# Performance work log

Measured on AMD Instinct MI355X. Metric: run time of the kernel, lower is better.

Reference implementation:

```python
import jax, jax.numpy as jnp
import numpy as np

ATOM_FDIM = 133
BOND_FDIM = 147
HIDDEN = 300
DEPTH = 3
N_ATOMS = 100000
N_BONDS = 200000
MAX_NB = 6
N_MOLS = 4000


def setup_inputs() -> dict:
    key = jax.random.key(0)
    ks = jax.random.split(key, 10)
    f_atoms = jax.random.normal(ks[0], (N_ATOMS, ATOM_FDIM), dtype=jnp.float32)
    f_bonds = jax.random.normal(ks[1], (N_BONDS, BOND_FDIM), dtype=jnp.float32)
    a2b = jax.random.randint(ks[2], (N_ATOMS, MAX_NB), 0, N_BONDS)
    b2a = jax.random.randint(ks[3], (N_BONDS,), 0, N_ATOMS)
    b2revb = jax.random.randint(ks[4], (N_BONDS,), 0, N_BONDS)
    atom2mol = jnp.sort(jax.random.randint(ks[5], (N_ATOMS,), 0, N_MOLS))
    s = 1.0 / np.sqrt(HIDDEN)
    W_i = jax.random.uniform(ks[6], (BOND_FDIM, HIDDEN), jnp.float32, -s, s)
    W_h = jax.random.uniform(ks[7], (HIDDEN, HIDDEN), jnp.float32, -s, s)
    W_o_w = jax.random.uniform(ks[8], (ATOM_FDIM + HIDDEN, HIDDEN), jnp.float32, -s, s)
    W_o_b = jax.random.uniform(ks[9], (HIDDEN,), jnp.float32, -s, s)
    return {"f_atoms": f_atoms, "f_bonds": f_bonds, "a2b": a2b, "b2a": b2a,
            "b2revb": b2revb, "atom2mol": atom2mol, "W_i": W_i, "W_h": W_h,
            "W_o_w": W_o_w, "W_o_b": W_o_b}


def reference(f_atoms, f_bonds, a2b, b2a, b2revb, atom2mol, W_i, W_h, W_o_w, W_o_b):
    # input = W_i(f_bonds); message = act(input)
    inp = f_bonds @ W_i                      # [n_bonds, hidden]
    message = jax.nn.relu(inp)
    for _ in range(DEPTH - 1):
        # gather neighbor bond messages per atom and sum: [n_atoms, max_nb, h] -> [n_atoms, h]
        a_message = message[a2b].sum(axis=1)
        rev_message = message[b2revb]        # [n_bonds, hidden]
        message = a_message[b2a] - rev_message
        message = jax.nn.relu(inp + message @ W_h)
    # final atom-level aggregation
    a_message = message[a2b].sum(axis=1)     # [n_atoms, hidden]
    a_input = jnp.concatenate([f_atoms, a_message], axis=1)
    atom_hiddens = jax.nn.relu(a_input @ W_o_w + W_o_b)
    # segment mean pooling over molecules
    sums = jax.ops.segment_sum(atom_hiddens, atom2mol, num_segments=N_MOLS)
    counts = jax.ops.segment_sum(jnp.ones((atom_hiddens.shape[0],), atom_hiddens.dtype),
                                 atom2mol, num_segments=N_MOLS)
    mol_vecs = sums / jnp.maximum(counts, 1.0)[:, None]  # zero vec for empty mols
    return mol_vecs
```

## Files before the change

kernel.cpp:

```cpp
#include <hip/hip_runtime.h>
#include <stdint.h>

#define ATOM_FDIM 133
#define BOND_FDIM 147
#define HIDDEN    300
#define N_ATOMS   100000
#define N_BONDS   200000
#define MAX_NB    6
#define N_MOLS    4000

#define KP_I 160
#define KP_H 320
#define KP_O 448
#define LDA  304
#define CPR  38

#define TM   128
#define ACH  8
#define BCH  20

typedef unsigned short u16;
typedef short bf16x8 __attribute__((ext_vector_type(8)));
typedef float f32x4 __attribute__((ext_vector_type(4)));

__device__ __forceinline__ u16 f2bu(float f) {
    unsigned u = __float_as_uint(f);
    u += 0x7FFFu + ((u >> 16) & 1u);
    return (u16)(u >> 16);
}
__device__ __forceinline__ float bu2f(u16 b) { return __uint_as_float(((unsigned)b) << 16); }

__device__ __forceinline__ uint4 relu_bf16x8(uint4 v) {
    union { uint4 u; u16 s[8]; } x, o;
    x.u = v;
    #pragma unroll
    for (int e = 0; e < 8; ++e) o.s[e] = (x.s[e] & 0x8000u) ? (u16)0 : x.s[e];
    return o.u;
}
__device__ __forceinline__ uint4 comb_bf16x8(uint4 vi, uint4 va, uint4 vy) {
    union { uint4 u; u16 s[8]; } xi, xa, xy, o;
    xi.u = vi; xa.u = va; xy.u = vy;
    #pragma unroll
    for (int e = 0; e < 8; ++e)
        o.s[e] = f2bu(fmaxf(bu2f(xi.s[e]) + bu2f(xa.s[e]) - bu2f(xy.s[e]), 0.f));
    return o.u;
}

#define AS1 __attribute__((address_space(1)))
#define AS3 __attribute__((address_space(3)))
__device__ __forceinline__ void gl_lds(const void* g, void* l) {
    __builtin_amdgcn_global_load_lds((const AS1 void*)g, (AS3 void*)l, 16, 0, 0);
}

template <int AM, int EPI>
__global__ __launch_bounds__(512, 2) void mm_k(
    const u16* __restrict__ A, int lda,
    const u16* __restrict__ aYp,
    const u16* __restrict__ Yp,
    const int* __restrict__ b2a,
    const int* __restrict__ b2revb,
    const u16* __restrict__ Wp,
    const float* __restrict__ bias,
    u16* __restrict__ out0, int ldo0,
    int M, int NT)
{
    __shared__ __align__(16) u16 As[2][ACH * 512];
    __shared__ __align__(16) u16 Bs[3][BCH * 512];

    const int t    = threadIdx.x;
    const int lane = t & 63, wid = t >> 6;
    const int fl   = lane & 15, fh = lane >> 4;
    const int m0   = blockIdx.x * TM;
    const int wr   = wid >> 1, wc = wid & 1;

    int arow = m0 + wid * 16 + fl;
    if (arow > M - 1) arow = M - 1;
    const char* pI = (const char*)A + (size_t)arow * (size_t)lda * 2u + (size_t)(fh * 16);
    const char* pA = nullptr; const char* pY = nullptr;
    if constexpr (AM == 2) {
        const int ia = b2a[arow], ir = b2revb[arow];
        pA = (const char*)aYp + (size_t)ia * (LDA * 2) + (size_t)(fh * 16);
        pY = (const char*)Yp  + (size_t)ir * (LDA * 2) + (size_t)(fh * 16);
    }
    const char* WpC = (const char*)Wp;
    const int bbase = (wid < 4) ? 3 * wid : 12 + 2 * (wid - 4);
    const size_t srcB0 = (size_t)bbase * 1024u + (size_t)lane * 16u;

    f32x4 acc[2][10] = {};
    uint4 Xi, Xa, Xy, Yi, Ya, Yy;
    (void)Xa; (void)Xy; (void)Ya; (void)Yy;

    Xi = *reinterpret_cast<const uint4*>(pI);
    if constexpr (AM == 2) { Xa = *reinterpret_cast<const uint4*>(pA);
                             Xy = *reinterpret_cast<const uint4*>(pY); }
    gl_lds(WpC + srcB0, (char*)Bs[0] + bbase * 1024);
    gl_lds(WpC + srcB0 + 1024, (char*)Bs[0] + bbase * 1024 + 1024);
    if (wid < 4) gl_lds(WpC + srcB0 + 2048, (char*)Bs[0] + bbase * 1024 + 2048);
    Yi = *reinterpret_cast<const uint4*>(pI + 64);
    if constexpr (AM == 2) { Ya = *reinterpret_cast<const uint4*>(pA + 64);
                             Yy = *reinterpret_cast<const uint4*>(pY + 64); }
    {
        const size_t kb1 = (size_t)(BCH * 1024);
        gl_lds(WpC + kb1 + srcB0, (char*)Bs[1] + bbase * 1024);
        gl_lds(WpC + kb1 + srcB0 + 1024, (char*)Bs[1] + bbase * 1024 + 1024);
        if (wid < 4) gl_lds(WpC + kb1 + srcB0 + 2048, (char*)Bs[1] + bbase * 1024 + 2048);
    }
    if constexpr (AM == 2) {
        if (wid < 4) asm volatile("s_waitcnt vmcnt(9)" ::: "memory");
        else         asm volatile("s_waitcnt vmcnt(7)" ::: "memory");
    } else {
        if (wid < 4) asm volatile("s_waitcnt vmcnt(7)" ::: "memory");
        else         asm volatile("s_waitcnt vmcnt(5)" ::: "memory");
    }
    {
        uint4 w0;
        if constexpr (AM == 2) w0 = comb_bf16x8(Xi, Xa, Xy);
        else if constexpr (AM == 1) w0 = relu_bf16x8(Xi);
        else w0 = Xi;
        *reinterpret_cast<uint4*>(&As[0][wid * 512 + lane * 8]) = w0;
    }
    if constexpr (AM == 2) {
        if (wid < 4) asm volatile("s_waitcnt vmcnt(6)" ::: "memory");
        else         asm volatile("s_waitcnt vmcnt(5)" ::: "memory");
    } else {
        if (wid < 4) asm volatile("s_waitcnt vmcnt(4)" ::: "memory");
        else         asm volatile("s_waitcnt vmcnt(3)" ::: "memory");
    }
    asm volatile("s_waitcnt lgkmcnt(0)" ::: "memory");
    __builtin_amdgcn_s_barrier();

    int tt = 0, bcur = 0;

#define GATE() do {                                                        \
    if constexpr (AM == 2) {                                               \
        if (wid < 4) asm volatile("s_waitcnt vmcnt(6)" ::: "memory");      \
        else         asm volatile("s_waitcnt vmcnt(5)" ::: "memory");      \
    } else {                                                               \
        if (wid < 4) asm volatile("s_waitcnt vmcnt(4)" ::: "memory");      \
        else         asm volatile("s_waitcnt vmcnt(3)" ::: "memory");      \
    } } while (0)

#define STEP(LI, LA, LY, WI, WA, WY) do {                                                   \
    int w2 = tt + 2; if (w2 >= NT) w2 -= NT;                                                \
    const u16* as_c = As[tt & 1];                                                           \
    const u16* bs_c = Bs[bcur];                                                             \
    int bnx = bcur + 2; if (bnx >= 3) bnx -= 3;                                             \
    char* bdst = (char*)Bs[bnx] + bbase * 1024;                                             \
    const size_t kbB = (size_t)w2 * (size_t)(BCH * 1024);                                   \
    bf16x8 af0, af1, bfv[10];                                                               \
    af0 = *reinterpret_cast<const bf16x8*>(&as_c[(wr * 2 + 0) * 512 + lane * 8]);           \
    af1 = *reinterpret_cast<const bf16x8*>(&as_c[(wr * 2 + 1) * 512 + lane * 8]);           \
    _Pragma("unroll")                                                                       \
    for (int n = 0; n < 5; ++n)                                                             \
        bfv[n] = *reinterpret_cast<const bf16x8*>(&bs_c[(wc * 10 + n) * 512 + lane * 8]);   \
    LI = *reinterpret_cast<const uint4*>(pI + (size_t)w2 * 64u);                            \
    if constexpr (AM == 2) {                                                                \
        LA = *reinterpret_cast<const uint4*>(pA + (size_t)w2 * 64u);                        \
        LY = *reinterpret_cast<const uint4*>(pY + (size_t)w2 * 64u);                        \
    }                                                                                       \
    gl_lds(WpC + kbB + srcB0, bdst);                                                        \
    __builtin_amdgcn_s_barrier();                                                           \
    __builtin_amdgcn_s_setprio(1);                                                          \
    _Pragma("unroll")                                                                       \
    for (int n = 0; n < 5; ++n) {                                                           \
        acc[0][n] = __builtin_amdgcn_mfma_f32_16x16x32_bf16(af0, bfv[n], acc[0][n], 0,0,0); \
        acc[1][n] = __builtin_amdgcn_mfma_f32_16x16x32_bf16(af1, bfv[n], acc[1][n], 0,0,0); \
    }                                                                                       \
    __builtin_amdgcn_s_setprio(0);                                                          \
    __builtin_amdgcn_s_barrier();                                                           \
    _Pragma("unroll")                                                                       \
    for (int n = 5; n < 10; ++n)                                                            \
        bfv[n] = *reinterpret_cast<const bf16x8*>(&bs_c[(wc * 10 + n) * 512 + lane * 8]);   \
    gl_lds(WpC + kbB + srcB0 + 1024, bdst + 1024);                                          \
    if (wid < 4) gl_lds(WpC + kbB + srcB0 + 2048, bdst + 2048);                             \
    GATE();                                                                                 \
    {                                                                                       \
        uint4 wv;                                                                           \
        if constexpr (AM == 2) wv = comb_bf16x8(WI, WA, WY);                                \
        else if constexpr (AM == 1) wv = relu_bf16x8(WI);                                   \
        else wv = WI;                                                                       \
        *reinterpret_cast<uint4*>(&As[(tt + 1) & 1][wid * 512 + lane * 8]) = wv;            \
    }                                                                                       \
    asm volatile("s_waitcnt lgkmcnt(0)" ::: "memory");                                      \
    __builtin_amdgcn_s_barrier();                                                           \
    __builtin_amdgcn_s_setprio(1);                                                          \
    _Pragma("unroll")                                                                       \
    for (int n = 5; n < 10; ++n) {                                                          \
        acc[0][n] = __builtin_amdgcn_mfma_f32_16x16x32_bf16(af0, bfv[n], acc[0][n], 0,0,0); \
        acc[1][n] = __builtin_amdgcn_mfma_f32_16x16x32_bf16(af1, bfv[n], acc[1][n], 0,0,0); \
    }                                                                                       \
    __builtin_amdgcn_s_setprio(0);                                                          \
    __builtin_amdgcn_s_barrier();                                                           \
    ++tt; bcur = (bcur == 2) ? 0 : bcur + 1;                                                \
} while (0)

    while (tt + 1 < NT) {
        STEP(Xi, Xa, Xy, Yi, Ya, Yy);
        STEP(Yi, Ya, Yy, Xi, Xa, Xy);
    }
    if (tt < NT) STEP(Xi, Xa, Xy, Yi, Ya, Yy);
#undef STEP
#undef GATE

    #pragma unroll
    for (int m = 0; m < 2; ++m) {
        #pragma unroll
        for (int r = 0; r < 4; ++r) {
            const int row = m0 + wr * 32 + m * 16 + fh * 4 + r;
            if (row >= M) continue;
            #pragma unroll
            for (int n = 0; n < 10; ++n) {
                const int col = wc * 160 + n * 16 + fl;
                if (col >= HIDDEN) continue;
                const float v = acc[m][n][r];
                if (EPI == 0) out0[(size_t)row * ldo0 + col] = f2bu(v);
                else          out0[(size_t)row * ldo0 + col] = f2bu(fmaxf(v + bias[col], 0.f));
            }
        }
    }
}

__global__ __launch_bounds__(256) void wconv_k(const float* __restrict__ W,
                                               int split, int off1, int Ktot, int NT,
                                               u16* __restrict__ Wp)
{
    const int id = blockIdx.x * 256 + threadIdx.x;
    if (id >= NT * BCH * 512) return;
    const int block = id >> 9, rem = id & 511;
    const int l = rem >> 3, e = rem & 7;
    const int c = block % BCH, kt = block / BCH;
    const int col = c * 16 + (l & 15);
    const int k   = kt * 32 + (l >> 4) * 8 + e;
    float v = 0.f;
    if (col < HIDDEN) {
        if (k < split) {
            const int r = k + off1;
            if (r < Ktot) v = W[(size_t)r * HIDDEN + col];
        } else {
            const int r = k - split;
            if (r < off1) v = W[(size_t)r * HIDDEN + col];
        }
    }
    Wp[id] = f2bu(v);
}

__global__ __launch_bounds__(256) void fbconv_k(const float* __restrict__ fb, u16* __restrict__ dst)
{
    const int id = blockIdx.x * 256 + threadIdx.x;
    if (id >= N_BONDS * KP_I) return;
    const int r = id / KP_I, k = id - r * KP_I;
    dst[id] = f2bu(k < BOND_FDIM ? fb[(size_t)r * BOND_FDIM + k] : 0.f);
}

__global__ __launch_bounds__(256) void agg_k(const u16* __restrict__ src,
                                             const int* __restrict__ a2b,
                                             u16* __restrict__ dst)
{
    const int c = blockIdx.x * 256 + threadIdx.x;
    if (c >= N_ATOMS * CPR) return;
    const int a = c / CPR, q = c - a * CPR;
    const int h = q * 8;
    const int* nb = a2b + (size_t)a * MAX_NB;
    float s[8] = {};
    #pragma unroll
    for (int j = 0; j < MAX_NB; ++j) {
        const int r = nb[j];
        union { uint4 u; u16 s[8]; } x;
        x.u = *(const uint4*)(src + (size_t)r * LDA + h);
        #pragma unroll
        for (int e = 0; e < 8; ++e) s[e] += bu2f(x.s[e]);
    }
    union { uint4 u; u16 s[8]; } o;
    #pragma unroll
    for (int e = 0; e < 8; ++e) o.s[e] = f2bu(s[e]);
    *(uint4*)(dst + (size_t)a * LDA + h) = o.u;
}

__global__ __launch_bounds__(256) void comb_k(const u16* __restrict__ inp,
                                              const u16* __restrict__ aY,
                                              const u16* __restrict__ Y,
                                              const int* __restrict__ b2a,
                                              const int* __restrict__ b2revb,
                                              u16* __restrict__ msg)
{
    const int c = blockIdx.x * 256 + threadIdx.x;
    if (c >= N_BONDS * CPR) return;
    const int b = c / CPR, q = c - b * CPR;
    const int h = q * 8;
    const int ia = b2a[b], ir = b2revb[b];
    union { uint4 u; u16 s[8]; } xi, xa, xy, o;
    xi.u = *(const uint4*)(inp + (size_t)b * LDA + h);
    xa.u = *(const uint4*)(aY + (size_t)ia * LDA + h);
    xy.u = *(const uint4*)(Y + (size_t)ir * LDA + h);
    #pragma unroll
    for (int j = 0; j < 8; ++j)
        o.s[j] = f2bu(fmaxf(bu2f(xi.s[j]) + bu2f(xa.s[j]) - bu2f(xy.s[j]), 0.f));
    *(uint4*)(msg + (size_t)b * LDA + h) = o.u;
}

__global__ __launch_bounds__(256) void aggcat_k(const u16* __restrict__ msg,
                                                const int* __restrict__ a2b,
                                                const float* __restrict__ fa,
                                                u16* __restrict__ dst)
{
    const int id = blockIdx.x * 256 + threadIdx.x;
    if (id >= N_ATOMS * (KP_O / 4)) return;
    const int a = id / (KP_O / 4), c = id - a * (KP_O / 4);
    const int e0 = c * 4;
    union { uint2 u; u16 s[4]; } o;
    if (e0 < HIDDEN) {
        const int* nb = a2b + (size_t)a * MAX_NB;
        float s0 = 0.f, s1 = 0.f, s2 = 0.f, s3 = 0.f;
        #pragma unroll
        for (int j = 0; j < MAX_NB; ++j) {
            union { uint2 u; u16 s[4]; } x;
            x.u = *(const uint2*)(msg + (size_t)nb[j] * LDA + e0);
            s0 += bu2f(x.s[0]); s1 += bu2f(x.s[1]); s2 += bu2f(x.s[2]); s3 += bu2f(x.s[3]);
        }
        o.s[0] = f2bu(s0); o.s[1] = f2bu(s1); o.s[2] = f2bu(s2); o.s[3] = f2bu(s3);
    } else {
        #pragma unroll
        for (int j = 0; j < 4; ++j) {
            const int fi = e0 + j - HIDDEN;
            o.s[j] = (fi < ATOM_FDIM) ? f2bu(fa[(size_t)a * ATOM_FDIM + fi]) : (u16)0;
        }
    }
    *(uint2*)(dst + (size_t)a * KP_O + e0) = o.u;
}

__global__ __launch_bounds__(320) void pool_k(const u16* __restrict__ ah,
                                              const int* __restrict__ a2m,
                                              float* __restrict__ out)
{
    const int m = blockIdx.x;
    int lo, hi;
    { int l = 0, r = N_ATOMS;
      while (l < r) { int mid = (l + r) >> 1; if (a2m[mid] < m) l = mid + 1; else r = mid; }
      lo = l; }
    { int l = lo, r = N_ATOMS;
      while (l < r) { int mid = (l + r) >> 1; if (a2m[mid] < m + 1) l = mid + 1; else r = mid; }
      hi = l; }
    const float inv = 1.0f / (float)((hi - lo) > 1 ? (hi - lo) : 1);
    const int h = threadIdx.x;
    if (h >= HIDDEN) return;
    float s = 0.f;
    for (int a = lo; a < hi; ++a) s += bu2f(ah[(size_t)a * LDA + h]);
    out[(size_t)m * HIDDEN + h] = s * inv;
}

extern "C" void kernel_launch(void* const* d_in, const int* in_sizes, int n_in,
                              void* d_out, int out_size, void* d_ws, size_t ws_size,
                              hipStream_t stream)
{
    const float* f_atoms  = (const float*)d_in[0];
    const float* f_bonds  = (const float*)d_in[1];
    const int*   a2b      = (const int*)d_in[2];
    const int*   b2a      = (const int*)d_in[3];
    const int*   b2revb   = (const int*)d_in[4];
    const int*   atom2mol = (const int*)d_in[5];
    const float* W_i      = (const float*)d_in[6];
    const float* W_h      = (const float*)d_in[7];
    const float* W_o_w    = (const float*)d_in[8];
    const float* W_o_b    = (const float*)d_in[9];
    float* out = (float*)d_out;

    char* p = (char*)d_ws;
    auto alloc = [&](size_t bytes) { char* r = p; p += (bytes + 255) & ~(size_t)255; return r; };
    u16* B0 = (u16*)alloc(((size_t)N_BONDS + 16) * LDA * 2);
    u16* B1 = (u16*)alloc(((size_t)N_BONDS + 16) * LDA * 2);
    u16* B2 = (u16*)alloc(((size_t)N_BONDS + 16) * LDA * 2);
    u16* aY = (u16*)alloc(((size_t)N_ATOMS + 16) * LDA * 2);
    u16* Wpi = (u16*)alloc((size_t)(KP_I / 32) * BCH * 512 * 2);
    u16* Wph = (u16*)alloc((size_t)(KP_H / 32) * BCH * 512 * 2);
    u16* Wpo = (u16*)alloc((size_t)(KP_O / 32) * BCH * 512 * 2);
    if ((size_t)(p - (char*)d_ws) > ws_size) return;

    u16* inp    = B0;
    u16* fb16   = B1;
    u16* Y1     = B1;
    u16* Y2     = B2;
    u16* msg2   = B1;
    u16* concat = B2;
    u16* ah     = B0;

    const dim3 blk(256);
    auto g1 = [](long long n) { return dim3((unsigned)((n + 255) / 256)); };
    const dim3 blk5(512);
    const dim3 gB((N_BONDS + TM - 1) / TM);
    const dim3 gA((N_ATOMS + TM - 1) / TM);

    const int BIGSPLIT = 1 << 20;
    wconv_k<<<g1((long long)(KP_I / 32) * BCH * 512), blk, 0, stream>>>(
        W_i, BIGSPLIT, 0, BOND_FDIM, KP_I / 32, Wpi);
    wconv_k<<<g1((long long)(KP_H / 32) * BCH * 512), blk, 0, stream>>>(
        W_h, BIGSPLIT, 0, HIDDEN, KP_H / 32, Wph);
    wconv_k<<<g1((long long)(KP_O / 32) * BCH * 512), blk, 0, stream>>>(
        W_o_w, HIDDEN, ATOM_FDIM, ATOM_FDIM + HIDDEN, KP_O / 32, Wpo);
    fbconv_k<<<g1((long long)N_BONDS * KP_I), blk, 0, stream>>>(f_bonds, fb16);

    mm_k<0, 0><<<gB, blk5, 0, stream>>>(fb16, KP_I, nullptr, nullptr, nullptr, nullptr,
                                        Wpi, nullptr, inp, LDA, N_BONDS, KP_I / 32);

    mm_k<1, 0><<<gB, blk5, 0, stream>>>(inp, LDA, nullptr, nullptr, nullptr, nullptr,
                                        Wph, nullptr, Y1, LDA, N_BONDS, KP_H / 32);
    agg_k<<<g1((long long)N_ATOMS * CPR), blk, 0, stream>>>(Y1, a2b, aY);

    mm_k<2, 0><<<gB, blk5, 0, stream>>>(inp, LDA, aY, Y1, b2a, b2revb,
                                        Wph, nullptr, Y2, LDA, N_BONDS, KP_H / 32);
    agg_k<<<g1((long long)N_ATOMS * CPR), blk, 0, stream>>>(Y2, a2b, aY);

    comb_k<<<g1((long long)N_BONDS * CPR), blk, 0, stream>>>(inp, aY, Y2, b2a, b2revb, msg2);
    aggcat_k<<<g1((long long)N_ATOMS * (KP_O / 4)), blk, 0, stream>>>(msg2, a2b, f_atoms, concat);

    mm_k<0, 1><<<gA, blk5, 0, stream>>>(concat, KP_O, nullptr, nullptr, nullptr, nullptr,
                                        Wpo, W_o_b, ah, LDA, N_ATOMS, KP_O / 32);
    pool_k<<<dim3(N_MOLS), dim3(320), 0, stream>>>(ah, atom2mol, out);
}
```

Baseline: 844.6 us.

## Add direct-to-LDS triple-buffered GEMM kernel for untransformed A operands

Splits the GEMM into two kernels. Plain GEMMs (input projection and output layer) now stream A tiles directly into LDS via global_load_lds with a three-stage ring buffer and a two-tile prefetch distance. This removes the register round-trip and the per-step LDS stores for A. The fused variant that applies relu or the message combine on A is kept for the hidden-layer GEMMs. The cost is more LDS per block and redundant wrapped prefetches in the last iterations.

Result: no change. 840.1 us (-0.5%).

```diff
diff --git a/kernel.cpp b/kernel.cpp
--- a/kernel.cpp
+++ b/kernel.cpp
@@ -52,15 +52,125 @@
     __builtin_amdgcn_global_load_lds((const AS1 void*)g, (AS3 void*)l, 16, 0, 0);
 }
 
-template <int AM, int EPI>
+template <int EPI>
 __global__ __launch_bounds__(512, 2) void mm_k(
+    const u16* __restrict__ A, int lda,
+    const u16* __restrict__ Wp,
+    const float* __restrict__ bias,
+    u16* __restrict__ out0, int ldo0,
+    int M, int NT)
+{
+    __shared__ __align__(16) u16 As[3][ACH * 512];
+    __shared__ __align__(16) u16 Bs[3][BCH * 512];
+
+    const int t    = threadIdx.x;
+    const int lane = t & 63, wid = t >> 6;
+    const int fl   = lane & 15, fh = lane >> 4;
+    const int m0   = blockIdx.x * TM;
+    const int wr   = wid >> 1, wc = wid & 1;
+
+    int arow = m0 + wid * 16 + fl;
+    if (arow > M - 1) arow = M - 1;
+    const char* srcAp = (const char*)A + (size_t)arow * (size_t)lda * 2u + (size_t)(fh * 16);
+    const char* WpC = (const char*)Wp;
+    const int bbase = (wid < 4) ? 3 * wid : 12 + 2 * (wid - 4);
+    const size_t srcB0 = (size_t)bbase * 1024u + (size_t)lane * 16u;
+
+    f32x4 acc[2][10] = {};
+
+#define STAGE_T(kt, buf) do {                                                    \
+        const size_t kbB_ = (size_t)(kt) * (size_t)(BCH * 1024);                 \
+        gl_lds(srcAp + (size_t)(kt) * 64u, (char*)As[buf] + wid * 1024);         \
+        gl_lds(WpC + kbB_ + srcB0,        (char*)Bs[buf] + bbase * 1024);        \
+        gl_lds(WpC + kbB_ + srcB0 + 1024, (char*)Bs[buf] + bbase * 1024 + 1024); \
+        if (wid < 4)                                                             \
+            gl_lds(WpC + kbB_ + srcB0 + 2048, (char*)Bs[buf] + bbase * 1024 + 2048); \
+    } while (0)
+
+#define GATE() do {                                                        \
+        if (wid < 4) asm volatile("s_waitcnt vmcnt(4)" ::: "memory");      \
+        else         asm volatile("s_waitcnt vmcnt(3)" ::: "memory");      \
+    } while (0)
+
+    STAGE_T(0, 0);
+    STAGE_T(1, 1);
+    GATE();
+    __builtin_amdgcn_s_barrier();
+
+    int cur = 0;
+    for (int tt = 0; tt < NT; ++tt) {
+        int w2 = tt + 2; if (w2 >= NT) w2 -= NT;
+        const int nx1 = (cur < 2) ? cur + 1 : 0;
+        const int nx2 = (nx1 < 2) ? nx1 + 1 : 0;
+        const u16* as_c = As[cur];
+        const u16* bs_c = Bs[cur];
+        const size_t kbB = (size_t)w2 * (size_t)(BCH * 1024);
+
+        bf16x8 af0, af1, bfv[10];
+        af0 = *reinterpret_cast<const bf16x8*>(&as_c[(wr * 2 + 0) * 512 + lane * 8]);
+        af1 = *reinterpret_cast<const bf16x8*>(&as_c[(wr * 2 + 1) * 512 + lane * 8]);
+        #pragma unroll
+        for (int n = 0; n < 5; ++n)
+            bfv[n] = *reinterpret_cast<const bf16x8*>(&bs_c[(wc * 10 + n) * 512 + lane * 8]);
+        gl_lds(srcAp + (size_t)w2 * 64u, (char*)As[nx2] + wid * 1024);
+        gl_lds(WpC + kbB + srcB0, (char*)Bs[nx2] + bbase * 1024);
+        __builtin_amdgcn_s_barrier();
+        __builtin_amdgcn_s_setprio(1);
+        #pragma unroll
+        for (int n = 0; n < 5; ++n) {
+            acc[0][n] = __builtin_amdgcn_mfma_f32_16x16x32_bf16(af0, bfv[n], acc[0][n], 0, 0, 0);
+            acc[1][n] = __builtin_amdgcn_mfma_f32_16x16x32_bf16(af1, bfv[n], acc[1][n], 0, 0, 0);
+        }
+        __builtin_amdgcn_s_setprio(0);
+        __builtin_amdgcn_s_barrier();
+
+        #pragma unroll
+        for (int n = 5; n < 10; ++n)
+            bfv[n] = *reinterpret_cast<const bf16x8*>(&bs_c[(wc * 10 + n) * 512 + lane * 8]);
+        gl_lds(WpC + kbB + srcB0 + 1024, (char*)Bs[nx2] + bbase * 1024 + 1024);
+        if (wid < 4)
+            gl_lds(WpC + kbB + srcB0 + 2048, (char*)Bs[nx2] + bbase * 1024 + 2048);
+        GATE();
+        __builtin_amdgcn_s_barrier();
+        __builtin_amdgcn_s_setprio(1);
+        #pragma unroll
+        for (int n = 5; n < 10; ++n) {
+            acc[0][n] = __builtin_amdgcn_mfma_f32_16x16x32_bf16(af0, bfv[n], acc[0][n], 0, 0, 0);
+            acc[1][n] = __builtin_amdgcn_mfma_f32_16x16x32_bf16(af1, bfv[n], acc[1][n], 0, 0, 0);
+        }
+        __builtin_amdgcn_s_setprio(0);
+        __builtin_amdgcn_s_barrier();
+        cur = nx1;
+    }
+#undef STAGE_T
+#undef GATE
+
+    #pragma unroll
+    for (int m = 0; m < 2; ++m) {
+        #pragma unroll
+        for (int r = 0; r < 4; ++r) {
+            const int row = m0 + wr * 32 + m * 16 + fh * 4 + r;
+            if (row >= M) continue;
+            #pragma unroll
+            for (int n = 0; n < 10; ++n) {
+                const int col = wc * 160 + n * 16 + fl;
+                if (col >= HIDDEN) continue;
+                const float v = acc[m][n][r];
+                if (EPI == 1) out0[(size_t)row * ldo0 + col] = f2bu(v);
+                else          out0[(size_t)row * ldo0 + col] = f2bu(fmaxf(v + bias[col], 0.f));
+            }
+        }
+    }
+}
+
+template <int AM>
+__global__ __launch_bounds__(512, 2) void mmf_k(
     const u16* __restrict__ A, int lda,
     const u16* __restrict__ aYp,
     const u16* __restrict__ Yp,
     const int* __restrict__ b2a,
     const int* __restrict__ b2revb,
     const u16* __restrict__ Wp,
-    const float* __restrict__ bias,
     u16* __restrict__ out0, int ldo0,
     int M, int NT)
 {
@@ -115,8 +225,7 @@
     {
         uint4 w0;
         if constexpr (AM == 2) w0 = comb_bf16x8(Xi, Xa, Xy);
-        else if constexpr (AM == 1) w0 = relu_bf16x8(Xi);
-        else w0 = Xi;
+        else                   w0 = relu_bf16x8(Xi);
         *reinterpret_cast<uint4*>(&As[0][wid * 512 + lane * 8]) = w0;
     }
     if constexpr (AM == 2) {
@@ -177,8 +286,7 @@
     {                                                                                       \
         uint4 wv;                                                                           \
         if constexpr (AM == 2) wv = comb_bf16x8(WI, WA, WY);                                \
-        else if constexpr (AM == 1) wv = relu_bf16x8(WI);                                   \
-        else wv = WI;                                                                       \
+        else                   wv = relu_bf16x8(WI);                                        \
         *reinterpret_cast<uint4*>(&As[(tt + 1) & 1][wid * 512 + lane * 8]) = wv;            \
     }                                                                                       \
     asm volatile("s_waitcnt lgkmcnt(0)" ::: "memory");                                      \
@@ -212,9 +320,7 @@
             for (int n = 0; n < 10; ++n) {
                 const int col = wc * 160 + n * 16 + fl;
                 if (col >= HIDDEN) continue;
-                const float v = acc[m][n][r];
-                if (EPI == 0) out0[(size_t)row * ldo0 + col] = f2bu(v);
-                else          out0[(size_t)row * ldo0 + col] = f2bu(fmaxf(v + bias[col], 0.f));
+                out0[(size_t)row * ldo0 + col] = f2bu(acc[m][n][r]);
             }
         }
     }
@@ -398,21 +504,21 @@
         W_o_w, HIDDEN, ATOM_FDIM, ATOM_FDIM + HIDDEN, KP_O / 32, Wpo);
     fbconv_k<<<g1((long long)N_BONDS * KP_I), blk, 0, stream>>>(f_bonds, fb16);
 
-    mm_k<0, 0><<<gB, blk5, 0, stream>>>(fb16, KP_I, nullptr, nullptr, nullptr, nullptr,
-                                        Wpi, nullptr, inp, LDA, N_BONDS, KP_I / 32);
-
-    mm_k<1, 0><<<gB, blk5, 0, stream>>>(inp, LDA, nullptr, nullptr, nullptr, nullptr,
-                                        Wph, nullptr, Y1, LDA, N_BONDS, KP_H / 32);
+    mm_k<1><<<gB, blk5, 0, stream>>>(fb16, KP_I, Wpi, nullptr,
+                                     inp, LDA, N_BONDS, KP_I / 32);
+
+    mmf_k<1><<<gB, blk5, 0, stream>>>(inp, LDA, nullptr, nullptr, nullptr, nullptr,
+                                      Wph, Y1, LDA, N_BONDS, KP_H / 32);
     agg_k<<<g1((long long)N_ATOMS * CPR), blk, 0, stream>>>(Y1, a2b, aY);
 
-    mm_k<2, 0><<<gB, blk5, 0, stream>>>(inp, LDA, aY, Y1, b2a, b2revb,
-                                        Wph, nullptr, Y2, LDA, N_BONDS, KP_H / 32);
+    mmf_k<2><<<gB, blk5, 0, stream>>>(inp, LDA, aY, Y1, b2a, b2revb,
+                                      Wph, Y2, LDA, N_BONDS, KP_H / 32);
     agg_k<<<g1((long long)N_ATOMS * CPR), blk, 0, stream>>>(Y2, a2b, aY);
 
     comb_k<<<g1((long long)N_BONDS * CPR), blk, 0, stream>>>(inp, aY, Y2, b2a, b2revb, msg2);
     aggcat_k<<<g1((long long)N_ATOMS * (KP_O / 4)), blk, 0, stream>>>(msg2, a2b, f_atoms, concat);
 
-    mm_k<0, 1><<<gA, blk5, 0, stream>>>(concat, KP_O, nullptr, nullptr, nullptr, nullptr,
-                                        Wpo, W_o_b, ah, LDA, N_ATOMS, KP_O / 32);
+    mm_k<2><<<gA, blk5, 0, stream>>>(concat, KP_O, Wpo, W_o_b,
+                                     ah, LDA, N_ATOMS, KP_O / 32);
     pool_k<<<dim3(N_MOLS), dim3(320), 0, stream>>>(ah, atom2mol, out);
 }
```
